# Performance work log

Hardware: AMD Instinct MI355X
Metric: run time of the kernel (lower is better)

The kernel has to match this reference:

```python
import jax, jax.numpy as jnp
import numpy as np

L, B, D, H, M, F = 384, 16, 1024, 16, 64, 4096
HD = D // H
LEFT, RIGHT = 64, 64
STD_SCALE = 0.5
LN_EPS = 1e-5


def layer_norm(x, w, b):
    mu = jnp.mean(x, axis=-1, keepdims=True)
    var = jnp.mean((x - mu) ** 2, axis=-1, keepdims=True)
    return (x - mu) / jnp.sqrt(var + LN_EPS) * w + b


def linear(x, w, b):  # torch nn.Linear: y = x @ W^T + b, w is [out, in]
    return x @ w.T + b


def attention_suppression(aw, scale):
    # aw: [N, Tq, Tk] raw logits (may contain -inf)
    p = jax.nn.softmax(aw, axis=-1)
    nz = p > 0.0  # entries with -inf logits are exactly 0 after softmax
    nzs = jnp.sum(nz.astype(aw.dtype), axis=-1, keepdims=True)
    mean = jnp.sum(p, axis=-1, keepdims=True) / nzs
    dis = jnp.where(nz, (p - mean) ** 2, jnp.zeros_like(p))
    var = jnp.sum(dis, axis=-1, keepdims=True) / (nzs - 1.0)
    thr = mean - scale * jnp.sqrt(var)
    return jnp.where(p < thr, -jnp.inf, aw)


def setup_inputs() -> dict:
    key = jax.random.key(0)
    ks = jax.random.split(key, 24)
    s = 0.02

    def w(k, shape):
        return jax.random.normal(k, shape, dtype=jnp.float32) * s

    return {
        "x": jax.random.normal(ks[0], (L, B, D), dtype=jnp.float32),
        "memory": jax.random.normal(ks[1], (M, B, D), dtype=jnp.float32),
        "q_w": w(ks[2], (D, D)), "q_b": jnp.zeros((D,), jnp.float32),
        "k_w": w(ks[3], (D, D)), "k_b": jnp.zeros((D,), jnp.float32),
        "v_w": w(ks[4], (D, D)), "v_b": jnp.zeros((D,), jnp.float32),
        "out_w": w(ks[5], (D, D)), "out_b": jnp.zeros((D,), jnp.float32),
        "ln1_w": jnp.ones((D,), jnp.float32), "ln1_b": jnp.zeros((D,), jnp.float32),
        "fc1_w": w(ks[6], (F, D)), "fc1_b": jnp.zeros((F,), jnp.float32),
        "fc2_w": w(ks[7], (D, F)), "fc2_b": jnp.zeros((D,), jnp.float32),
        "ln2_w": jnp.ones((D,), jnp.float32), "ln2_b": jnp.zeros((D,), jnp.float32),
    }


def reference(x, memory, q_w, q_b, k_w, k_b, v_w, v_b, out_w, out_b,
              ln1_w, ln1_b, fc1_w, fc1_b, fc2_w, fc2_b, ln2_w, ln2_b):
    residual = x
    xn = layer_norm(x, ln1_w, ln1_b)  # normalize_before
    # summarization query = mean over segment (excluding left/right context)
    summary = jnp.mean(xn[LEFT:L - RIGHT], axis=0, keepdims=True)  # [1,B,D]
    inp = jnp.concatenate([xn, summary], axis=0)  # [L+1, B, D]
    mem_and_inp = jnp.concatenate([memory, inp[:-1]], axis=0)  # [M+L, B, D]

    scaling = HD ** -0.5
    q = linear(inp, q_w, q_b) * scaling
    k = linear(mem_and_inp, k_w, k_b)
    v = linear(mem_and_inp, v_w, v_b)

    def split_heads(t):  # [T,B,D] -> [B*H, T, HD]
        return t.reshape(t.shape[0], B * H, HD).transpose(1, 0, 2)

    q, k, v = split_heads(q), split_heads(k), split_heads(v)
    aw = jnp.einsum('nqd,nkd->nqk', q, k)  # [B*H, L+1, M+L]
    # disable mem-on-mem: summary (last) query must not attend to memory keys
    aw = aw.at[:, -1, :M].set(-jnp.inf)
    aw = attention_suppression(aw, STD_SCALE)
    p = jax.nn.softmax(aw, axis=-1)
    attn = jnp.einsum('nqk,nkd->nqd', p, v)  # [B*H, L+1, HD]
    attn = attn.transpose(1, 0, 2).reshape(L + 1, B, D)
    out_and_mem = linear(attn, out_w, out_b)
    # next_m = out_and_mem[-1:] appended to state (identity squash); output drops it
    out = out_and_mem[:-1]

    x = residual + out
    residual = x
    xn = layer_norm(x, ln2_w, ln2_b)
    h = jax.nn.relu(linear(xn, fc1_w, fc1_b))
    h = linear(h, fc2_w, fc2_b)
    return residual + h
```

## Files before the change

kernel.cpp:

```cpp
#include <hip/hip_runtime.h>

typedef __bf16 bf16x8 __attribute__((ext_vector_type(8)));
typedef float f32x4 __attribute__((ext_vector_type(4)));
typedef unsigned short u16x8 __attribute__((ext_vector_type(8)));

__device__ __forceinline__ unsigned short f2bf(float f) {
  union { float f; unsigned int u; } v; v.f = f;
  unsigned int r = v.u + 0x7fffu + ((v.u >> 16) & 1u);
  return (unsigned short)(r >> 16);
}

__device__ __forceinline__ void async16(const unsigned short* g, unsigned short* l) {
  __builtin_amdgcn_global_load_lds(
      (const __attribute__((address_space(1))) unsigned int*)g,
      (__attribute__((address_space(3))) unsigned int*)l, 16, 0, 0);
}

__global__ void cvt_bf16(const float* __restrict__ s, unsigned short* __restrict__ d, int n4,
                         float scale) {
  int i = blockIdx.x * 256 + threadIdx.x;
  if (i >= n4) return;
  float4 v = ((const float4*)s)[i];
  ushort4 o;
  o.x = f2bf(v.x * scale); o.y = f2bf(v.y * scale);
  o.z = f2bf(v.z * scale); o.w = f2bf(v.w * scale);
  ((ushort4*)d)[i] = o;
}

__global__ void concat_bias(const float* __restrict__ qb, const float* __restrict__ kb,
                            const float* __restrict__ vb, float* __restrict__ o) {
  int i = blockIdx.x * 256 + threadIdx.x;
  float v = (i < 1024) ? qb[i] * 0.125f : (i < 2048 ? kb[i - 1024] : vb[i - 2048]);
  o[i] = v;
}

template <int PREFILL>
__global__ __launch_bounds__(256) void ln_bf16(
    const float* __restrict__ src, unsigned short* __restrict__ dst,
    const float* __restrict__ g, const float* __restrict__ be,
    const float* __restrict__ fbias, float* __restrict__ dout) {
  const int row = blockIdx.x, tid = threadIdx.x;
  const float4 v = ((const float4*)(src + (size_t)row * 1024))[tid];
  if (PREFILL) {
    const float4 fb = ((const float4*)fbias)[tid];
    float4 r;
    r.x = v.x + fb.x; r.y = v.y + fb.y; r.z = v.z + fb.z; r.w = v.w + fb.w;
    ((float4*)(dout + (size_t)row * 1024))[tid] = r;
  }
  float s = v.x + v.y + v.z + v.w;
  float qq = v.x * v.x + v.y * v.y + v.z * v.z + v.w * v.w;
#pragma unroll
  for (int off = 32; off; off >>= 1) { s += __shfl_xor(s, off); qq += __shfl_xor(qq, off); }
  __shared__ float ps[4], pq[4];
  const int w = tid >> 6, lane = tid & 63;
  if (lane == 0) { ps[w] = s; pq[w] = qq; }
  __syncthreads();
  if (tid == 0) { ps[0] = ps[0] + ps[1] + ps[2] + ps[3]; pq[0] = pq[0] + pq[1] + pq[2] + pq[3]; }
  __syncthreads();
  const float mu = ps[0] * (1.f / 1024.f);
  const float var = pq[0] * (1.f / 1024.f) - mu * mu;
  const float rs = rsqrtf(var + 1e-5f);
  const float4 gv = ((const float4*)g)[tid];
  const float4 bv = ((const float4*)be)[tid];
  ushort4 o;
  o.x = f2bf((v.x - mu) * rs * gv.x + bv.x);
  o.y = f2bf((v.y - mu) * rs * gv.y + bv.y);
  o.z = f2bf((v.z - mu) * rs * gv.z + bv.z);
  o.w = f2bf((v.w - mu) * rs * gv.w + bv.w);
  ((ushort4*)(dst + (size_t)row * 1024))[tid] = o;
}

#define KOFF 6291456ull
#define VOFF 13631488ull
template <int EPI>
__global__ __launch_bounds__(256) void gemm_bt(
    const unsigned short* __restrict__ A, const unsigned short* __restrict__ Bw,
    const float* __restrict__ bias, const float* __restrict__ resid,
    void* __restrict__ Cout, int M, int N, int K, int lda, int ldb) {
  __shared__ __align__(16) unsigned short lA[128 * 32];
  __shared__ __align__(16) unsigned short lB[128 * 32];
  const int tid = threadIdx.x;
  const int w = tid >> 6, lane = tid & 63;
  const int lr = lane & 15, lq = lane >> 4;
  const int bm = blockIdx.y, bn = blockIdx.x;
  const size_t koff = (size_t)blockIdx.z * K;
  const unsigned short* Ab = A + (size_t)bm * 128 * lda + koff;
  const unsigned short* Bb = Bw + (size_t)bn * 128 * ldb + koff;
  const int wm = (w & 1) << 6, wn = (w >> 1) << 6;
  f32x4 acc[4][4] = {};
  const int kiters = K >> 5;
  const int c0 = tid, c1 = 256 + tid;
  const int r0 = c0 >> 2, o0 = (c0 & 3) << 3;
  const int r1 = c1 >> 2, o1 = (c1 & 3) << 3;
  for (int kt = 0; kt < kiters; ++kt) {
    const int kb = kt << 5;
    __syncthreads();
    async16(Ab + (size_t)r0 * lda + kb + o0, lA + c0 * 8);
    async16(Bb + (size_t)r0 * ldb + kb + o0, lB + c0 * 8);
    async16(Ab + (size_t)r1 * lda + kb + o1, lA + c1 * 8);
    async16(Bb + (size_t)r1 * ldb + kb + o1, lB + c1 * 8);
    __syncthreads();
    bf16x8 af[4], bfr[4];
#pragma unroll
    for (int i = 0; i < 4; ++i) af[i] = *(const bf16x8*)(lA + (wm + i * 16 + lr) * 32 + lq * 8);
#pragma unroll
    for (int i = 0; i < 4; ++i) bfr[i] = *(const bf16x8*)(lB + (wn + i * 16 + lr) * 32 + lq * 8);
#pragma unroll
    for (int i = 0; i < 4; ++i)
#pragma unroll
      for (int j = 0; j < 4; ++j)
        acc[i][j] = __builtin_amdgcn_mfma_f32_16x16x32_bf16(af[i], bfr[j], acc[i][j], 0, 0, 0);
  }
  const int which = (bn * 128) >> 10;
#pragma unroll
  for (int i = 0; i < 4; ++i) {
#pragma unroll
    for (int j = 0; j < 4; ++j) {
      const int colg = bn * 128 + wn + j * 16 + lr;
      const float bi = (EPI == 6) ? 0.f : bias[colg];
      const int rowg0 = bm * 128 + wm + i * 16 + lq * 4;
#pragma unroll
      for (int r = 0; r < 4; ++r) {
        const int rowg = rowg0 + r;
        const float val = acc[i][j][r] + bi;
        if (EPI == 5) {
          const int t = rowg >> 4, bb = rowg & 15;
          const int hh = (colg >> 6) & 15, dd = colg & 63;
          const size_t nn = (size_t)(bb * 16 + hh);
          unsigned short* q16 = (unsigned short*)Cout;
          if (which == 0) {
            if (rowg >= 1024) q16[(nn * 384 + (t - 64)) * 64 + dd] = f2bf(val);
          } else if (which == 1) {
            q16[KOFF + (nn * 448 + t) * 64 + dd] = f2bf(val);
          } else {
            q16[VOFF + (nn * 448 + t) * 64 + dd] = f2bf(val);
          }
        } else {
          const size_t idx = (size_t)rowg * N + colg;
          if (EPI == 2) ((float*)Cout)[idx] = val + resid[idx];
          else if (EPI == 3) ((unsigned short*)Cout)[idx] = f2bf(fmaxf(val, 0.f));
          else if (EPI == 6) atomicAdd(&((float*)Cout)[idx], acc[i][j][r]);
        }
      }
    }
  }
}

__global__ __launch_bounds__(256) void vtrans(const unsigned short* __restrict__ vb,
                                              unsigned short* __restrict__ vt) {
  __shared__ __align__(16) unsigned short ls[64][80];
  const int kc = blockIdx.x, n = blockIdx.y;
  const int tid = threadIdx.x;
#pragma unroll
  for (int i = 0; i < 2; ++i) {
    const int c = i * 256 + tid;
    const int kk = c >> 3, dc = (c & 7) << 3;
    u16x8 val = *(const u16x8*)(vb + ((size_t)n * 448 + kc * 64 + kk) * 64 + dc);
    *(u16x8*)&ls[kk][dc] = val;
  }
  __syncthreads();
#pragma unroll
  for (int i = 0; i < 2; ++i) {
    const int c = i * 256 + tid;
    const int d = c >> 3, kx = (c & 7) << 3;
    u16x8 o;
#pragma unroll
    for (int j = 0; j < 8; ++j) o[j] = ls[kx + j][d];
    *(u16x8*)(vt + ((size_t)n * 64 + d) * 448 + kc * 64 + kx) = o;
  }
}

#define PST 468
__global__ __launch_bounds__(256) void attn_kernel(
    const unsigned short* __restrict__ qt_, const unsigned short* __restrict__ kt_,
    const unsigned short* __restrict__ vt_, unsigned short* __restrict__ attn) {
  __shared__ __align__(16) unsigned short P[16 * PST];
  __shared__ float Rm[4][16], Rs[4][16], Rc[4][16], Rv[4][16], R2[4][16];
  __shared__ __align__(16) float OT[4][16][17];
  const int id = blockIdx.x;
  const int xcd = id & 7, j0 = id >> 3;
  const int n = xcd * 32 + (j0 & 31), qt = j0 >> 5;
  const int b = n >> 4, h = n & 15;
  const int tid = threadIdx.x, w = tid >> 6, lane = tid & 63;
  const int lr = lane & 15, lq = lane >> 4;

  const unsigned short* qp = qt_ + ((size_t)n * 384 + qt * 16 + lr) * 64 + lq * 8;
  const bf16x8 q0 = *(const bf16x8*)qp;
  const bf16x8 q1 = *(const bf16x8*)(qp + 32);

  f32x4 acc[7];
#pragma unroll
  for (int t = 0; t < 7; ++t) {
    const unsigned short* kp = kt_ + ((size_t)n * 448 + (w * 7 + t) * 16 + lr) * 64 + lq * 8;
    const bf16x8 k0 = *(const bf16x8*)kp;
    const bf16x8 k1 = *(const bf16x8*)(kp + 32);
    f32x4 a = {0.f, 0.f, 0.f, 0.f};
    a = __builtin_amdgcn_mfma_f32_16x16x32_bf16(k0, q0, a, 0, 0, 0);
    a = __builtin_amdgcn_mfma_f32_16x16x32_bf16(k1, q1, a, 0, 0, 0);
    acc[t] = a;
  }

  f32x4 m4 = acc[0];
#pragma unroll
  for (int t = 1; t < 7; ++t) {
    m4[0] = fmaxf(m4[0], acc[t][0]); m4[1] = fmaxf(m4[1], acc[t][1]);
    m4[2] = fmaxf(m4[2], acc[t][2]); m4[3] = fmaxf(m4[3], acc[t][3]);
  }
  float m = fmaxf(fmaxf(m4[0], m4[1]), fmaxf(m4[2], m4[3]));
  m = fmaxf(m, __shfl_xor(m, 16));
  m = fmaxf(m, __shfl_xor(m, 32));
  if (lq == 0) Rm[w][lr] = m;
  __syncthreads();
  m = fmaxf(fmaxf(Rm[0][lr], Rm[1][lr]), fmaxf(Rm[2][lr], Rm[3][lr]));

  f32x4 s4 = {0.f, 0.f, 0.f, 0.f}, c4 = {0.f, 0.f, 0.f, 0.f};
#pragma unroll
  for (int t = 0; t < 7; ++t) {
#pragma unroll
    for (int r = 0; r < 4; ++r) {
      const float e = __expf(acc[t][r] - m);
      acc[t][r] = e;
      s4[r] += e;
      if (e > 0.f) c4[r] += 1.f;
    }
  }
  float s = (s4[0] + s4[1]) + (s4[2] + s4[3]);
  float cnt = (c4[0] + c4[1]) + (c4[2] + c4[3]);
  s += __shfl_xor(s, 16); s += __shfl_xor(s, 32);
  cnt += __shfl_xor(cnt, 16); cnt += __shfl_xor(cnt, 32);
  if (lq == 0) { Rs[w][lr] = s; Rc[w][lr] = cnt; }
  __syncthreads();
  s = (Rs[0][lr] + Rs[1][lr]) + (Rs[2][lr] + Rs[3][lr]);
  cnt = (Rc[0][lr] + Rc[1][lr]) + (Rc[2][lr] + Rc[3][lr]);
  const float inv = 1.f / s;
  const float mean = 1.f / cnt;

  f32x4 d4 = {0.f, 0.f, 0.f, 0.f};
#pragma unroll
  for (int t = 0; t < 7; ++t) {
#pragma unroll
    for (int r = 0; r < 4; ++r) {
      const float p = acc[t][r] * inv;
      const float dd = p - mean;
      if (acc[t][r] > 0.f) d4[r] += dd * dd;
    }
  }
  float dv = (d4[0] + d4[1]) + (d4[2] + d4[3]);
  dv += __shfl_xor(dv, 16); dv += __shfl_xor(dv, 32);
  if (lq == 0) Rv[w][lr] = dv;
  __syncthreads();
  dv = (Rv[0][lr] + Rv[1][lr]) + (Rv[2][lr] + Rv[3][lr]);
  const float thr = mean - 0.5f * sqrtf(dv / (cnt - 1.f));

  f32x4 t4 = {0.f, 0.f, 0.f, 0.f};
#pragma unroll
  for (int t = 0; t < 7; ++t) {
#pragma unroll
    for (int r = 0; r < 4; ++r) {
      if (!(acc[t][r] * inv < thr)) t4[r] += acc[t][r];
    }
  }
  float s2 = (t4[0] + t4[1]) + (t4[2] + t4[3]);
  s2 += __shfl_xor(s2, 16); s2 += __shfl_xor(s2, 32);
  if (lq == 0) R2[w][lr] = s2;
  __syncthreads();
  s2 = (R2[0][lr] + R2[1][lr]) + (R2[2][lr] + R2[3][lr]);
  const float inv2 = 1.f / s2;

#pragma unroll
  for (int t = 0; t < 7; ++t) {
#pragma unroll
    for (int rp = 0; rp < 4; rp += 2) {
      const float v0 = (acc[t][rp] * inv < thr) ? 0.f : acc[t][rp] * inv2;
      const float v1 = (acc[t][rp + 1] * inv < thr) ? 0.f : acc[t][rp + 1] * inv2;
      const unsigned int u = (unsigned int)f2bf(v0) | ((unsigned int)f2bf(v1) << 16);
      *(unsigned int*)&P[lr * PST + (w * 7 + t) * 16 + lq * 4 + rp] = u;
    }
  }
  __syncthreads();

  f32x4 o = {0.f, 0.f, 0.f, 0.f};
#pragma unroll
  for (int c = 0; c < 14; ++c) {
    union { ushort4 hh[2]; bf16x8 v; } bf;
    bf.hh[0] = *(const ushort4*)&P[lr * PST + c * 32 + lq * 8];
    bf.hh[1] = *(const ushort4*)&P[lr * PST + c * 32 + lq * 8 + 4];
    const bf16x8 a = *(const bf16x8*)(vt_ + ((size_t)n * 64 + w * 16 + lr) * 448 + c * 32 + lq * 8);
    o = __builtin_amdgcn_mfma_f32_16x16x32_bf16(a, bf.v, o, 0, 0, 0);
  }

#pragma unroll
  for (int r = 0; r < 4; ++r) OT[w][lq * 4 + r][lr] = o[r];
  const int qrow = lane >> 2, dg = lane & 3;
  ushort4 ov;
  ov.x = f2bf(OT[w][dg * 4 + 0][qrow]);
  ov.y = f2bf(OT[w][dg * 4 + 1][qrow]);
  ov.z = f2bf(OT[w][dg * 4 + 2][qrow]);
  ov.w = f2bf(OT[w][dg * 4 + 3][qrow]);
  *(ushort4*)(attn + ((size_t)(qt * 16 + qrow) * 16 + b) * 1024 + h * 64 + w * 16 + dg * 4) = ov;
}

extern "C" void kernel_launch(void* const* d_in, const int* in_sizes, int n_in,
                              void* d_out, int out_size, void* d_ws, size_t ws_size,
                              hipStream_t stream) {
  (void)in_sizes; (void)n_in; (void)out_size; (void)ws_size;
  const float* x    = (const float*)d_in[0];
  const float* mem  = (const float*)d_in[1];
  const float* q_w  = (const float*)d_in[2];
  const float* q_b  = (const float*)d_in[3];
  const float* k_w  = (const float*)d_in[4];
  const float* k_b  = (const float*)d_in[5];
  const float* v_w  = (const float*)d_in[6];
  const float* v_b  = (const float*)d_in[7];
  const float* o_w  = (const float*)d_in[8];
  const float* o_b  = (const float*)d_in[9];
  const float* ln1w = (const float*)d_in[10];
  const float* ln1b = (const float*)d_in[11];
  const float* f1w  = (const float*)d_in[12];
  const float* f1b  = (const float*)d_in[13];
  const float* f2w  = (const float*)d_in[14];
  const float* f2b  = (const float*)d_in[15];
  const float* ln2w = (const float*)d_in[16];
  const float* ln2b = (const float*)d_in[17];

  unsigned short* WQ   = (unsigned short*)d_ws;
  unsigned short* WK   = WQ + 1048576;
  unsigned short* WV   = WK + 1048576;
  unsigned short* WO   = WV + 1048576;
  unsigned short* WF1  = WO + 1048576;
  unsigned short* WF2  = WF1 + 4194304;
  unsigned short* ABUF = WF2 + 4194304;
  unsigned short* QB   = ABUF + 7340032;
  unsigned short* KB   = QB + 6291456;
  unsigned short* VB   = KB + 7340032;
  unsigned short* VT   = VB + 7340032;
  unsigned short* ATTN = VT + 7340032;
  float*          X2   = (float*)(ATTN + 6291456);
  float*          QKVB = (float*)ATTN;
  unsigned short* XN2  = ATTN;
  unsigned short* HB   = ABUF;

  cvt_bf16<<<1024, 256, 0, stream>>>(q_w, WQ, 262144, 0.125f);
  cvt_bf16<<<1024, 256, 0, stream>>>(k_w, WK, 262144, 1.f);
  cvt_bf16<<<1024, 256, 0, stream>>>(v_w, WV, 262144, 1.f);
  cvt_bf16<<<1024, 256, 0, stream>>>(o_w, WO, 262144, 1.f);
  cvt_bf16<<<4096, 256, 0, stream>>>(f1w, WF1, 1048576, 1.f);
  cvt_bf16<<<4096, 256, 0, stream>>>(f2w, WF2, 1048576, 1.f);
  cvt_bf16<<<1024, 256, 0, stream>>>(mem, ABUF, 262144, 1.f);
  concat_bias<<<12, 256, 0, stream>>>(q_b, k_b, v_b, QKVB);

  ln_bf16<0><<<6144, 256, 0, stream>>>(x, ABUF + 1048576, ln1w, ln1b, nullptr, nullptr);

  gemm_bt<5><<<dim3(24, 56), 256, 0, stream>>>(ABUF, WQ, QKVB, nullptr, QB, 7168, 3072, 1024, 1024, 1024);

  vtrans<<<dim3(7, 256), 256, 0, stream>>>(VB, VT);
  attn_kernel<<<6144, 256, 0, stream>>>(QB, KB, VT, ATTN);

  gemm_bt<2><<<dim3(8, 48), 256, 0, stream>>>(ATTN, WO, o_b, x, X2, 6144, 1024, 1024, 1024, 1024);

  ln_bf16<1><<<6144, 256, 0, stream>>>(X2, XN2, ln2w, ln2b, f2b, (float*)d_out);

  gemm_bt<3><<<dim3(32, 48), 256, 0, stream>>>(XN2, WF1, f1b, nullptr, HB, 6144, 4096, 1024, 1024, 1024);
  gemm_bt<6><<<dim3(8, 48, 2), 256, 0, stream>>>(HB, WF2, nullptr, nullptr, d_out, 6144, 1024, 2048, 4096, 4096);
}
```

Baseline: 541.4 us.

## Remap GEMM tiles per XCD for L2 reuse and fuse conversion launches

Switches the GEMMs to a 1D grid and maps blocks so each of the 8 XCDs owns a contiguous set of N-column tiles. Blocks on the same XCD then share weight tiles in that XCD's L2. Separately, merges the seven weight/memory conversion kernels and the bias concat into one launch to cut launch overhead. The mapping assumes the hardware dispatches blocks round-robin across 8 XCDs, and it requires the N tile count to equal 8*W.

```diff
diff --git a/kernel.cpp b/kernel.cpp
--- a/kernel.cpp
+++ b/kernel.cpp
@@ -16,22 +16,36 @@
       (__attribute__((address_space(3))) unsigned int*)l, 16, 0, 0);
 }
 
-__global__ void cvt_bf16(const float* __restrict__ s, unsigned short* __restrict__ d, int n4,
-                         float scale) {
-  int i = blockIdx.x * 256 + threadIdx.x;
-  if (i >= n4) return;
-  float4 v = ((const float4*)s)[i];
+__global__ void cvt_all(const float* __restrict__ q_w, const float* __restrict__ k_w,
+                        const float* __restrict__ v_w, const float* __restrict__ o_w,
+                        const float* __restrict__ f1w, const float* __restrict__ f2w,
+                        const float* __restrict__ mem,
+                        const float* __restrict__ q_b, const float* __restrict__ k_b,
+                        const float* __restrict__ v_b,
+                        unsigned short* __restrict__ WQ, unsigned short* __restrict__ WK,
+                        unsigned short* __restrict__ WV, unsigned short* __restrict__ WO,
+                        unsigned short* __restrict__ WF1, unsigned short* __restrict__ WF2,
+                        unsigned short* __restrict__ MEMB, float* __restrict__ QKVB) {
+  const int bid = blockIdx.x;
+  const float* src; unsigned short* dst; float scale = 1.f; int base;
+  if (bid < 1024)       { src = q_w; dst = WQ;  scale = 0.125f; base = 0; }
+  else if (bid < 2048)  { src = k_w; dst = WK;  base = 1024; }
+  else if (bid < 3072)  { src = v_w; dst = WV;  base = 2048; }
+  else if (bid < 4096)  { src = o_w; dst = WO;  base = 3072; }
+  else if (bid < 8192)  { src = f1w; dst = WF1; base = 4096; }
+  else if (bid < 12288) { src = f2w; dst = WF2; base = 8192; }
+  else if (bid < 13312) { src = mem; dst = MEMB; base = 12288; }
+  else {
+    const int i = (bid - 13312) * 256 + threadIdx.x;
+    QKVB[i] = (i < 1024) ? q_b[i] * 0.125f : (i < 2048 ? k_b[i - 1024] : v_b[i - 2048]);
+    return;
+  }
+  const int i = (bid - base) * 256 + threadIdx.x;
+  float4 v = ((const float4*)src)[i];
   ushort4 o;
   o.x = f2bf(v.x * scale); o.y = f2bf(v.y * scale);
   o.z = f2bf(v.z * scale); o.w = f2bf(v.w * scale);
-  ((ushort4*)d)[i] = o;
-}
-
-__global__ void concat_bias(const float* __restrict__ qb, const float* __restrict__ kb,
-                            const float* __restrict__ vb, float* __restrict__ o) {
-  int i = blockIdx.x * 256 + threadIdx.x;
-  float v = (i < 1024) ? qb[i] * 0.125f : (i < 2048 ? kb[i - 1024] : vb[i - 2048]);
-  o[i] = v;
+  ((ushort4*)dst)[i] = o;
 }
 
 template <int PREFILL>
@@ -76,14 +90,18 @@
 __global__ __launch_bounds__(256) void gemm_bt(
     const unsigned short* __restrict__ A, const unsigned short* __restrict__ Bw,
     const float* __restrict__ bias, const float* __restrict__ resid,
-    void* __restrict__ Cout, int M, int N, int K, int lda, int ldb) {
+    void* __restrict__ Cout, int M, int N, int K, int lda, int ldb, int NBM, int W) {
   __shared__ __align__(16) unsigned short lA[128 * 32];
   __shared__ __align__(16) unsigned short lB[128 * 32];
   const int tid = threadIdx.x;
   const int w = tid >> 6, lane = tid & 63;
   const int lr = lane & 15, lq = lane >> 4;
-  const int bm = blockIdx.y, bn = blockIdx.x;
-  const size_t koff = (size_t)blockIdx.z * K;
+  const int l = blockIdx.x;
+  const int xcd = l & 7, r = l >> 3;
+  const int bn = xcd * W + (r % W);
+  const int rest = r / W;
+  const int bm = rest % NBM;
+  const size_t koff = (size_t)(rest / NBM) * K;
   const unsigned short* Ab = A + (size_t)bm * 128 * lda + koff;
   const unsigned short* Bb = Bw + (size_t)bn * 128 * ldb + koff;
   const int wm = (w & 1) << 6, wn = (w >> 1) << 6;
@@ -120,9 +138,9 @@
       const float bi = (EPI == 6) ? 0.f : bias[colg];
       const int rowg0 = bm * 128 + wm + i * 16 + lq * 4;
 #pragma unroll
-      for (int r = 0; r < 4; ++r) {
-        const int rowg = rowg0 + r;
-        const float val = acc[i][j][r] + bi;
+      for (int r2 = 0; r2 < 4; ++r2) {
+        const int rowg = rowg0 + r2;
+        const float val = acc[i][j][r2] + bi;
         if (EPI == 5) {
           const int t = rowg >> 4, bb = rowg & 15;
           const int hh = (colg >> 6) & 15, dd = colg & 63;
@@ -139,7 +157,7 @@
           const size_t idx = (size_t)rowg * N + colg;
           if (EPI == 2) ((float*)Cout)[idx] = val + resid[idx];
           else if (EPI == 3) ((unsigned short*)Cout)[idx] = f2bf(fmaxf(val, 0.f));
-          else if (EPI == 6) atomicAdd(&((float*)Cout)[idx], acc[i][j][r]);
+          else if (EPI == 6) atomicAdd(&((float*)Cout)[idx], acc[i][j][r2]);
         }
       }
     }
@@ -340,26 +358,20 @@
   unsigned short* XN2  = ATTN;
   unsigned short* HB   = ABUF;
 
-  cvt_bf16<<<1024, 256, 0, stream>>>(q_w, WQ, 262144, 0.125f);
-  cvt_bf16<<<1024, 256, 0, stream>>>(k_w, WK, 262144, 1.f);
-  cvt_bf16<<<1024, 256, 0, stream>>>(v_w, WV, 262144, 1.f);
-  cvt_bf16<<<1024, 256, 0, stream>>>(o_w, WO, 262144, 1.f);
-  cvt_bf16<<<4096, 256, 0, stream>>>(f1w, WF1, 1048576, 1.f);
-  cvt_bf16<<<4096, 256, 0, stream>>>(f2w, WF2, 1048576, 1.f);
-  cvt_bf16<<<1024, 256, 0, stream>>>(mem, ABUF, 262144, 1.f);
-  concat_bias<<<12, 256, 0, stream>>>(q_b, k_b, v_b, QKVB);
+  cvt_all<<<13324, 256, 0, stream>>>(q_w, k_w, v_w, o_w, f1w, f2w, mem, q_b, k_b, v_b,
+                                     WQ, WK, WV, WO, WF1, WF2, ABUF, QKVB);
 
   ln_bf16<0><<<6144, 256, 0, stream>>>(x, ABUF + 1048576, ln1w, ln1b, nullptr, nullptr);
 
-  gemm_bt<5><<<dim3(24, 56), 256, 0, stream>>>(ABUF, WQ, QKVB, nullptr, QB, 7168, 3072, 1024, 1024, 1024);
+  gemm_bt<5><<<1344, 256, 0, stream>>>(ABUF, WQ, QKVB, nullptr, QB, 7168, 3072, 1024, 1024, 1024, 56, 3);
 
   vtrans<<<dim3(7, 256), 256, 0, stream>>>(VB, VT);
   attn_kernel<<<6144, 256, 0, stream>>>(QB, KB, VT, ATTN);
 
-  gemm_bt<2><<<dim3(8, 48), 256, 0, stream>>>(ATTN, WO, o_b, x, X2, 6144, 1024, 1024, 1024, 1024);
+  gemm_bt<2><<<384, 256, 0, stream>>>(ATTN, WO, o_b, x, X2, 6144, 1024, 1024, 1024, 1024, 48, 1);
 
   ln_bf16<1><<<6144, 256, 0, stream>>>(X2, XN2, ln2w, ln2b, f2b, (float*)d_out);
 
-  gemm_bt<3><<<dim3(32, 48), 256, 0, stream>>>(XN2, WF1, f1b, nullptr, HB, 6144, 4096, 1024, 1024, 1024);
-  gemm_bt<6><<<dim3(8, 48, 2), 256, 0, stream>>>(HB, WF2, nullptr, nullptr, d_out, 6144, 1024, 2048, 4096, 4096);
-}
+  gemm_bt<3><<<1536, 256, 0, stream>>>(XN2, WF1, f1b, nullptr, HB, 6144, 4096, 1024, 1024, 1024, 48, 4);
+  gemm_bt<6><<<768, 256, 0, stream>>>(HB, WF2, nullptr, nullptr, d_out, 6144, 1024, 2048, 4096, 4096, 48, 1);
+}
```

After: 530.1 us. -2.1%, faster.
